# Kernel tuning notes

Measured on AMD Instinct MI355X. Metric: run time of the kernel, lower is better.

## Reference

```python
import jax, jax.numpy as jnp
import numpy as np

N_BITS = 8
IN_FEATURES = 2048
OUT_FEATURES = 512
BATCH = 8
THRESHOLD = 0.5


def setup_inputs() -> dict:
    key = jax.random.key(0)
    kx, kw = jax.random.split(key)
    x = jax.random.uniform(kx, (BATCH, IN_FEATURES), dtype=jnp.float32)
    # nn.init.normal_(weight, mean=0.5, std=1.0) then clamp_(0, 1)
    weight = 0.5 + jax.random.normal(kw, (IN_FEATURES, OUT_FEATURES * N_BITS), dtype=jnp.float32)
    weight = jnp.clip(weight, 0.0, 1.0)
    return {"x": x, "weight": weight}


def _carry_save_adder(addends):
    # addends: [M, F, n_bits] -> reduce over F via full-adder chain.
    # Bit index 0 = LSB; carry shifts one position toward MSB each step.
    M, F, nb = addends.shape
    a_seq = jnp.transpose(addends, (1, 0, 2))  # [F, M, nb]
    init = (jnp.zeros((M, nb), addends.dtype), jnp.zeros((M, nb), addends.dtype))

    def step(state, a):
        s, c = state
        t = s + a + c
        half = jnp.floor(t * 0.5)          # carry bit (zero-gradient)
        sum_b = t - 2.0 * half             # t mod 2 (identity gradient w.r.t. t)
        c_next = jnp.pad(half[:, :-1], ((0, 0), (1, 0)))  # shift-left: LSB carry-in = 0
        return (sum_b, c_next), None

    (s, c), _ = jax.lax.scan(step, init, a_seq)
    return s, c


def reference(x, weight):
    # STE binarization of the weights (forward value = hard bits)
    w = jnp.clip(weight, 0.0, 1.0)
    hard = w + jax.lax.stop_gradient((w >= THRESHOLD).astype(w.dtype) - w)
    # [B, F, 1] * [1, F, O*nb] -> [B, F, O*nb]
    ff = x[:, :, None] * hard[None, :, :]
    B, F, _ = ff.shape
    O = ff.shape[-1] // N_BITS
    # split(n_bits, dim=-1) + stack(dim=-3) + reshape -> [B*O, F, n_bits]
    stacked = ff.reshape(B, F, O, N_BITS).transpose(0, 2, 1, 3).reshape(B * O, F, N_BITS)
    s, carry = _carry_save_adder(stacked)   # [B*O, nb], [B*O, nb]
    s = s.reshape(B, N_BITS * O)
    return (s, carry)
```

## Files before the change

kernel.cpp:

```cpp
#include <hip/hip_runtime.h>


#define F_DIM 2048
#define K_DIM 4096
#define B_DIM 8
#define G     32
#define NG    (F_DIM / G)
#define NB2   4

#define PK_BYTES (64 * NG * 64 * 4)

__device__ __forceinline__ float dpp_row_shr1(float v) {
    int r = __builtin_amdgcn_update_dpp(0, __float_as_int(v), 0x111, 0xf, 0xf, true);
    return __int_as_float(r);
}

__device__ __forceinline__ int sext_bit(unsigned bits, int u) {
#if __has_builtin(__builtin_amdgcn_sbfe)
    return __builtin_amdgcn_sbfe((int)bits, (unsigned)u, 1u);
#else
    return ((int)(bits << (31 - u))) >> 31;
#endif
}

__global__ __launch_bounds__(64) void pack_kernel(const float* __restrict__ w,
                                                  unsigned* __restrict__ pk) {
    const int lane = threadIdx.x;
    const int og   = blockIdx.x;
    const int f32  = blockIdx.y;
    const float* wp = w + og * 64 + lane;
    unsigned bits = 0;
#pragma unroll
    for (int j = 0; j < 32; ++j) {
        float wv = wp[(f32 * 32 + j) * K_DIM];
        bits |= (wv >= 0.5f ? 1u : 0u) << j;
    }
    pk[(og * 64 + f32) * 64 + lane] = bits;
}

__global__ __launch_bounds__(64, 1) void csa_main(const float* __restrict__ x,
                                                  const unsigned* __restrict__ pk,
                                                  float* __restrict__ out) {
    const int lane = threadIdx.x;
    const int og   = blockIdx.x + 8 * blockIdx.y;
    const int b    = blockIdx.z;
    const int k    = og * 64 + lane;

    const float kmask = ((lane & 7) == 7) ? 0.0f : 1.0f;

    int zero;
    asm volatile("v_mov_b32 %0, 0" : "=v"(zero));

    const unsigned* bp  = pk + og * (NG * 64) + lane;
    const float4*   xp4 = (const float4*)(x + b * F_DIM) + zero;

    unsigned bbuf[NB2];
    float4   xb[NB2][G / 4];

#pragma unroll
    for (int p = 0; p < NB2; ++p) {
        bbuf[p] = bp[p * 64];
#pragma unroll
        for (int q = 0; q < G / 4; ++q)
            xb[p][q] = xp4[p * (G / 4) + q];
    }

    float s = 0.0f, c = 0.0f;

    for (int g0 = 0; g0 < NG; g0 += NB2) {
#pragma unroll
        for (int p = 0; p < NB2; ++p) {
            const float*   xf   = (const float*)&xb[p][0];
            const unsigned bits = bbuf[p];
#pragma unroll
            for (int u = 0; u < G; ++u) {
                int   m  = sext_bit(bits, u);
                float a  = __int_as_float(m & __float_as_int(xf[u]));
                float uu = s + a;
                float t  = uu + c;
                bool  ge = (t >= 2.0f);
                float h  = ge ? kmask : 0.0f;
                s = ge ? (t - 2.0f) : t;
                c = dpp_row_shr1(h);
            }
            int gb = g0 + p + NB2;
            int gc = (gb < NG) ? gb : (NG - 1);
            bbuf[p] = bp[gc * 64];
#pragma unroll
            for (int q = 0; q < G / 4; ++q)
                xb[p][q] = xp4[gc * (G / 4) + q];
        }
    }

    out[b * K_DIM + k]                 = s;
    out[B_DIM * K_DIM + b * K_DIM + k] = c;
}

#define U_FB  16
#define NB_FB 4
__global__ __launch_bounds__(64, 1) void csa_fallback(const float* __restrict__ x,
                                                      const float* __restrict__ weight,
                                                      float* __restrict__ out) {
    const int lane = threadIdx.x;
    const int og   = blockIdx.x + 8 * blockIdx.y;
    const int b    = blockIdx.z;
    const int k    = og * 64 + lane;
    const float kmask = ((lane & 7) == 7) ? 0.0f : 1.0f;
    int zero;
    asm volatile("v_mov_b32 %0, 0" : "=v"(zero));
    const float*  wp  = weight + k;
    const float4* xp4 = (const float4*)(x + b * F_DIM) + zero;
    float  wb[NB_FB][U_FB];
    float4 xb[NB_FB][U_FB / 4];
#pragma unroll
    for (int p = 0; p < NB_FB; ++p) {
#pragma unroll
        for (int u = 0; u < U_FB; ++u) wb[p][u] = wp[(p * U_FB + u) * K_DIM];
#pragma unroll
        for (int q = 0; q < U_FB / 4; ++q) xb[p][q] = xp4[(p * U_FB) / 4 + q];
    }
    float s = 0.0f, c = 0.0f;
    for (int f0 = 0; f0 < F_DIM; f0 += NB_FB * U_FB) {
#pragma unroll
        for (int p = 0; p < NB_FB; ++p) {
            const float* xf = (const float*)&xb[p][0];
#pragma unroll
            for (int u = 0; u < U_FB; ++u) {
                float a  = (wb[p][u] >= 0.5f) ? xf[u] : 0.0f;
                float uu = s + a;
                float t  = uu + c;
                bool  ge = (t >= 2.0f);
                float h  = ge ? kmask : 0.0f;
                s = ge ? (t - 2.0f) : t;
                c = dpp_row_shr1(h);
            }
            int fb = f0 + p * U_FB + NB_FB * U_FB;
            int fc = (fb <= F_DIM - U_FB) ? fb : (F_DIM - U_FB);
#pragma unroll
            for (int u = 0; u < U_FB; ++u) wb[p][u] = wp[(fc + u) * K_DIM];
#pragma unroll
            for (int q = 0; q < U_FB / 4; ++q) xb[p][q] = xp4[fc / 4 + q];
        }
    }
    out[b * K_DIM + k]                 = s;
    out[B_DIM * K_DIM + b * K_DIM + k] = c;
}

extern "C" void kernel_launch(void* const* d_in, const int* in_sizes, int n_in,
                              void* d_out, int out_size, void* d_ws, size_t ws_size,
                              hipStream_t stream) {
    (void)in_sizes; (void)n_in; (void)out_size;
    const float* x      = (const float*)d_in[0];
    const float* weight = (const float*)d_in[1];
    float* out          = (float*)d_out;

    if (ws_size >= (size_t)PK_BYTES && d_ws != nullptr) {
        unsigned* pk = (unsigned*)d_ws;
        pack_kernel<<<dim3(64, 64, 1), dim3(64), 0, stream>>>(weight, pk);
        csa_main<<<dim3(8, 8, 8), dim3(64), 0, stream>>>(x, pk, out);
    } else {
        csa_fallback<<<dim3(8, 8, 8), dim3(64), 0, stream>>>(x, weight, out);
    }
}
```

Baseline: 124.4 us.

## Vectorize weight packing with float4 loads and reformulate CSA step via floor/fma

The pack kernel now loads float4 per thread, so each thread builds four bit-words and writes them as one uint4, with a grid a quarter the size. The CSA inner loop swaps the compare/select sequence for a floor-based carry (floor(t*0.5)) and an fma for the sum. The carry mask moves to the receiving lane, applied via fma on the shifted raw carry, and the stored carry is masked at the end. This shortens the serial dependency chain per step and cuts pack-kernel load instructions, but it relies on the floor path matching the reference's floor semantics exactly.

```diff
diff --git a/kernel.cpp b/kernel.cpp
--- a/kernel.cpp
+++ b/kernel.cpp
@@ -25,17 +25,25 @@
 
 __global__ __launch_bounds__(64) void pack_kernel(const float* __restrict__ w,
                                                   unsigned* __restrict__ pk) {
-    const int lane = threadIdx.x;
-    const int og   = blockIdx.x;
-    const int f32  = blockIdx.y;
-    const float* wp = w + og * 64 + lane;
-    unsigned bits = 0;
+    const int t   = threadIdx.x;
+    const int ogq = blockIdx.x;
+    const int f32 = blockIdx.y;
+
+    const float4* w4 = (const float4*)(w + ogq * 256) + t;
+
+    unsigned b0 = 0, b1 = 0, b2 = 0, b3 = 0;
 #pragma unroll
     for (int j = 0; j < 32; ++j) {
-        float wv = wp[(f32 * 32 + j) * K_DIM];
-        bits |= (wv >= 0.5f ? 1u : 0u) << j;
+        float4 v = w4[(f32 * 32 + j) * (K_DIM / 4)];
+        b0 |= (v.x >= 0.5f ? 1u : 0u) << j;
+        b1 |= (v.y >= 0.5f ? 1u : 0u) << j;
+        b2 |= (v.z >= 0.5f ? 1u : 0u) << j;
+        b3 |= (v.w >= 0.5f ? 1u : 0u) << j;
     }
-    pk[(og * 64 + f32) * 64 + lane] = bits;
+    const int og  = ogq * 4 + (t >> 4);
+    const int col = (t & 15) * 4;
+    uint4* dst = (uint4*)(pk + (og * NG + f32) * 64 + col);
+    *dst = make_uint4(b0, b1, b2, b3);
 }
 
 __global__ __launch_bounds__(64, 1) void csa_main(const float* __restrict__ x,
@@ -46,7 +54,7 @@
     const int b    = blockIdx.z;
     const int k    = og * 64 + lane;
 
-    const float kmask = ((lane & 7) == 7) ? 0.0f : 1.0f;
+    const float lsbmask = ((lane & 7) == 0) ? 0.0f : 1.0f;
 
     int zero;
     asm volatile("v_mov_b32 %0, 0" : "=v"(zero));
@@ -65,7 +73,7 @@
             xb[p][q] = xp4[p * (G / 4) + q];
     }
 
-    float s = 0.0f, c = 0.0f;
+    float s = 0.0f, craw = 0.0f;
 
     for (int g0 = 0; g0 < NG; g0 += NB2) {
 #pragma unroll
@@ -77,11 +85,10 @@
                 int   m  = sext_bit(bits, u);
                 float a  = __int_as_float(m & __float_as_int(xf[u]));
                 float uu = s + a;
-                float t  = uu + c;
-                bool  ge = (t >= 2.0f);
-                float h  = ge ? kmask : 0.0f;
-                s = ge ? (t - 2.0f) : t;
-                c = dpp_row_shr1(h);
+                float t  = fmaf(craw, lsbmask, uu);
+                float h  = floorf(t * 0.5f);
+                s = fmaf(-2.0f, h, t);
+                craw = dpp_row_shr1(h);
             }
             int gb = g0 + p + NB2;
             int gc = (gb < NG) ? gb : (NG - 1);
@@ -93,7 +100,7 @@
     }
 
     out[b * K_DIM + k]                 = s;
-    out[B_DIM * K_DIM + b * K_DIM + k] = c;
+    out[B_DIM * K_DIM + b * K_DIM + k] = craw * lsbmask;
 }
 
 #define U_FB  16
@@ -105,7 +112,7 @@
     const int og   = blockIdx.x + 8 * blockIdx.y;
     const int b    = blockIdx.z;
     const int k    = og * 64 + lane;
-    const float kmask = ((lane & 7) == 7) ? 0.0f : 1.0f;
+    const float lsbmask = ((lane & 7) == 0) ? 0.0f : 1.0f;
     int zero;
     asm volatile("v_mov_b32 %0, 0" : "=v"(zero));
     const float*  wp  = weight + k;
@@ -119,7 +126,7 @@
 #pragma unroll
         for (int q = 0; q < U_FB / 4; ++q) xb[p][q] = xp4[(p * U_FB) / 4 + q];
     }
-    float s = 0.0f, c = 0.0f;
+    float s = 0.0f, craw = 0.0f;
     for (int f0 = 0; f0 < F_DIM; f0 += NB_FB * U_FB) {
 #pragma unroll
         for (int p = 0; p < NB_FB; ++p) {
@@ -128,11 +135,10 @@
             for (int u = 0; u < U_FB; ++u) {
                 float a  = (wb[p][u] >= 0.5f) ? xf[u] : 0.0f;
                 float uu = s + a;
-                float t  = uu + c;
-                bool  ge = (t >= 2.0f);
-                float h  = ge ? kmask : 0.0f;
-                s = ge ? (t - 2.0f) : t;
-                c = dpp_row_shr1(h);
+                float t  = fmaf(craw, lsbmask, uu);
+                float h  = floorf(t * 0.5f);
+                s = fmaf(-2.0f, h, t);
+                craw = dpp_row_shr1(h);
             }
             int fb = f0 + p * U_FB + NB_FB * U_FB;
             int fc = (fb <= F_DIM - U_FB) ? fb : (F_DIM - U_FB);
@@ -143,7 +149,7 @@
         }
     }
     out[b * K_DIM + k]                 = s;
-    out[B_DIM * K_DIM + b * K_DIM + k] = c;
+    out[B_DIM * K_DIM + b * K_DIM + k] = craw * lsbmask;
 }
 
 extern "C" void kernel_launch(void* const* d_in, const int* in_sizes, int n_in,
@@ -156,7 +162,7 @@
 
     if (ws_size >= (size_t)PK_BYTES && d_ws != nullptr) {
         unsigned* pk = (unsigned*)d_ws;
-        pack_kernel<<<dim3(64, 64, 1), dim3(64), 0, stream>>>(weight, pk);
+        pack_kernel<<<dim3(16, 64, 1), dim3(64), 0, stream>>>(weight, pk);
         csa_main<<<dim3(8, 8, 8), dim3(64), 0, stream>>>(x, pk, out);
     } else {
         csa_fallback<<<dim3(8, 8, 8), dim3(64), 0, stream>>>(x, weight, out);
```

Result: no change. 124.8 us (+0.3%).
